# Kernel tuning notes

Hardware: AMD Instinct MI355X
Metric: run time of the kernel (lower is better)

The kernel has to match this reference:

```python
import jax, jax.numpy as jnp
import numpy as np

A, B, I, J, K = 8, 256, 256, 256, 256  # a=batch, b=tokens, i=s-channels, j=c-channels, k=out_dim


def setup_inputs() -> dict:
    key = jax.random.key(0)
    k1, k2, k3 = jax.random.split(key, 3)
    input_s = jax.random.normal(k1, (A, B, I), dtype=jnp.float32)
    input_c = jax.random.normal(k2, (B, J), dtype=jnp.float32)
    # learned params: w ~ N(0, 0.02), b zeros (as in build())
    w = jax.random.normal(k3, (I, J, K), dtype=jnp.float32) * 0.02
    b = jnp.zeros((K,), dtype=jnp.float32)
    return {"input_s": input_s, "input_c": input_c, "w": w, "b": b}


def reference(input_s, input_c, w, b):
    # Original: tmp = einsum('abi,ijk->abjk', input_s, w); out = einsum('bj,abjk->abk', input_c, tmp) + b
    # Mathematically identical fused bilinear contraction (avoids the [a,b,j,k] intermediate):
    out = jnp.einsum('abi,bj,ijk->abk', input_s, input_c, w)
    return out + b
```

## Files before the change

### kernel.cpp

```cpp
#include <hip/hip_runtime.h>
#include <hip/hip_bf16.h>

#define A_ 8
#define B_ 256
#define I_ 256
#define J_ 256
#define K_ 256

typedef __attribute__((ext_vector_type(8))) short short8_t;
typedef __attribute__((ext_vector_type(4))) float f32x4_t;

static __device__ __forceinline__ uint pack2bf(float a, float b) {
  float2 f2; f2.x = a; f2.y = b;
  __hip_bfloat162 h2 = __float22bfloat162_rn(f2);
  uint r;
  __builtin_memcpy(&r, &h2, 4);
  return r;
}

static __device__ __forceinline__ ushort f2bf(float f) {
  __hip_bfloat16 h = __float2bfloat16(f);
  ushort us;
  __builtin_memcpy(&us, &h, 2);
  return us;
}

static __device__ __forceinline__ float bf2f(ushort h) {
  uint u = ((uint)h) << 16;
  float f;
  __builtin_memcpy(&f, &u, 4);
  return f;
}

__global__ __launch_bounds__(256) void prepass_c_kernel(
    const float* __restrict__ c, ushort* __restrict__ cbf) {
  const int idx = blockIdx.x * 256 + threadIdx.x;
  const f32x4_t v = *reinterpret_cast<const f32x4_t*>(c + (size_t)idx * 4);
  uint2 r;
  r.x = pack2bf(v[0], v[1]);
  r.y = pack2bf(v[2], v[3]);
  *reinterpret_cast<uint2*>(cbf + (size_t)idx * 4) = r;
}

#define LDK 40

__global__ __launch_bounds__(256, 3) void pass1_kernel(
    const ushort* __restrict__ cbf, const float* __restrict__ w,
    ushort* __restrict__ u) {
  const int i    = blockIdx.x;
  const int k0   = blockIdx.y * 64;
  const int tid  = threadIdx.x;
  const int lane = tid & 63;
  const int wave = tid >> 6;
  const int lrow = lane & 15;
  const int lhi  = lane >> 4;

  __shared__ ushort Bt[2][64][LDK];

  const float* wi = w + (size_t)i * (J_ * K_) + k0;

  const int jp = tid & 15;
  const int kq = tid >> 4;

  const int arow = wave * 64 + lrow;

  f32x4_t acc[4][4];
#pragma unroll
  for (int m = 0; m < 4; m++)
#pragma unroll
    for (int n = 0; n < 4; n++) acc[m][n] = (f32x4_t)(0.0f);

  f32x4_t  bv[2][2];
  short8_t afr[2][4];

#define BGLOB(p, t)                                                         \
  {                                                                         \
    _Pragma("unroll") for (int jj = 0; jj < 2; jj++)                        \
        bv[p][jj] = *reinterpret_cast<const f32x4_t*>(                      \
            wi + (size_t)((t) * 32 + jp * 2 + jj) * K_ + kq * 4);           \
  }
#define ALOAD(p, t)                                                         \
  {                                                                         \
    _Pragma("unroll") for (int m = 0; m < 4; m++)                           \
        afr[p][m] = *reinterpret_cast<const short8_t*>(                     \
            cbf + (size_t)(arow + m * 16) * J_ + (t) * 32 + lhi * 8);       \
  }
#define STOREB(buf, p)                                                      \
  {                                                                         \
    _Pragma("unroll") for (int kk = 0; kk < 4; kk++)                        \
        *reinterpret_cast<uint*>(&Bt[buf][kq * 4 + kk][jp * 2]) =           \
            pack2bf(bv[p][0][kk], bv[p][1][kk]);                            \
  }

  BGLOB(0, 0);
  BGLOB(1, 1);
  ALOAD(0, 0);
  ALOAD(1, 1);
  STOREB(0, 0);
  asm volatile("s_waitcnt lgkmcnt(0)" ::: "memory");
  __builtin_amdgcn_s_barrier();

#pragma unroll
  for (int t = 0; t < 8; ++t) {
    const int cur = t & 1;
    short8_t bfr[4];
#pragma unroll
    for (int n = 0; n < 4; n++)
      bfr[n] = *reinterpret_cast<const short8_t*>(
          &Bt[cur][n * 16 + lrow][lhi * 8]);
    if (t < 6) BGLOB(cur, t + 2);
#pragma unroll
    for (int m = 0; m < 4; m++)
#pragma unroll
      for (int n = 0; n < 4; n++)
        acc[m][n] = __builtin_amdgcn_mfma_f32_16x16x32_bf16(
            afr[cur][m], bfr[n], acc[m][n], 0, 0, 0);
    if (t < 6) ALOAD(cur, t + 2);
    if (t < 7) {
      STOREB(cur ^ 1, cur ^ 1);
      asm volatile("s_waitcnt lgkmcnt(0)" ::: "memory");
      __builtin_amdgcn_s_barrier();
    }
  }
#undef BGLOB
#undef ALOAD
#undef STOREB

#pragma unroll
  for (int m = 0; m < 4; m++) {
    const int brow = wave * 64 + m * 16 + lhi * 4;
#pragma unroll
    for (int n = 0; n < 4; n++) {
      const int kc = k0 + n * 16 + lrow;
      ushort* up = u + ((size_t)brow * I_ + i) * K_ + kc;
#pragma unroll
      for (int r = 0; r < 4; r++)
        up[(size_t)r * (I_ * K_)] = f2bf(acc[m][n][r]);
    }
  }
}

__global__ __launch_bounds__(256) void pass2_kernel(
    const float* __restrict__ s, const ushort* __restrict__ u,
    const float* __restrict__ bias, float* __restrict__ out) {
  const int b   = blockIdx.x;
  const int a0  = blockIdx.y * 4;
  const int tid = threadIdx.x;
  __shared__ float s_l[4][I_];
  __shared__ float red[8][4][K_];

#pragma unroll
  for (int v = 0; v < 4; v++) {
    const int idx = tid + v * 256;
    const int a = idx >> 8, ii = idx & 255;
    s_l[a][ii] = s[((size_t)(a0 + a) * B_ + b) * I_ + ii];
  }
  __syncthreads();

  const int kb = (tid & 31) * 8;
  const int ig = tid >> 5;
  float acc[4][8];
#pragma unroll
  for (int a = 0; a < 4; a++)
#pragma unroll
    for (int q = 0; q < 8; q++) acc[a][q] = 0.0f;

  const ushort* ub = u + ((size_t)b * I_ + ig * 32) * K_ + kb;
  for (int ii = 0; ii < 32; ++ii) {
    const short8_t uv = *reinterpret_cast<const short8_t*>(ub + (size_t)ii * K_);
    float f[8];
#pragma unroll
    for (int q = 0; q < 8; q++) f[q] = bf2f((ushort)uv[q]);
    const int i = ig * 32 + ii;
#pragma unroll
    for (int a = 0; a < 4; a++) {
      const float sa = s_l[a][i];
#pragma unroll
      for (int q = 0; q < 8; q++) acc[a][q] += sa * f[q];
    }
  }

#pragma unroll
  for (int a = 0; a < 4; a++) {
    f32x4_t r0, r1;
#pragma unroll
    for (int q = 0; q < 4; q++) { r0[q] = acc[a][q]; r1[q] = acc[a][4 + q]; }
    *reinterpret_cast<f32x4_t*>(&red[ig][a][kb])     = r0;
    *reinterpret_cast<f32x4_t*>(&red[ig][a][kb + 4]) = r1;
  }
  __syncthreads();

#pragma unroll
  for (int v = 0; v < 4; v++) {
    const int k = tid;
    float sum = 0.0f;
#pragma unroll
    for (int g = 0; g < 8; g++) sum += red[g][v][k];
    out[((size_t)(a0 + v) * B_ + b) * K_ + k] = sum + bias[k];
  }
}

__global__ __launch_bounds__(256) void fallback_kernel(
    const float* __restrict__ s, const float* __restrict__ cmat,
    const float* __restrict__ w, const float* __restrict__ bias,
    float* __restrict__ out) {
  const int b = blockIdx.x;
  const int k = threadIdx.x;
  __shared__ float c_l[J_];
  __shared__ float s_l[A_][I_];
  for (int idx = threadIdx.x; idx < J_; idx += 256) c_l[idx] = cmat[(size_t)b * J_ + idx];
  for (int idx = threadIdx.x; idx < A_ * I_; idx += 256) {
    const int a = idx >> 8;
    const int i = idx & 255;
    s_l[a][i] = s[(size_t)a * (B_ * I_) + (size_t)b * I_ + i];
  }
  __syncthreads();
  float acc[A_];
#pragma unroll
  for (int a = 0; a < A_; a++) acc[a] = 0.0f;
  for (int i = 0; i < I_; i++) {
    const float* wrow = w + (size_t)i * (J_ * K_) + k;
    float inner = 0.0f;
    for (int j = 0; j < J_; j++) inner += c_l[j] * wrow[(size_t)j * K_];
#pragma unroll
    for (int a = 0; a < A_; a++) acc[a] += s_l[a][i] * inner;
  }
#pragma unroll
  for (int a = 0; a < A_; a++)
    out[((size_t)a * B_ + b) * K_ + k] = acc[a] + bias[k];
}

extern "C" void kernel_launch(void* const* d_in, const int* in_sizes, int n_in,
                              void* d_out, int out_size, void* d_ws, size_t ws_size,
                              hipStream_t stream) {
  const float* s    = (const float*)d_in[0];
  const float* cmat = (const float*)d_in[1];
  const float* w    = (const float*)d_in[2];
  const float* bias = (const float*)d_in[3];
  float* out = (float*)d_out;

  const size_t u_elems   = (size_t)B_ * I_ * K_;
  const size_t cbf_elems = (size_t)B_ * J_;
  const size_t need = (u_elems + cbf_elems) * sizeof(ushort);

  if (ws_size >= need) {
    ushort* u   = (ushort*)d_ws;
    ushort* cbf = (ushort*)d_ws + u_elems;
    prepass_c_kernel<<<dim3((B_ * J_) / (256 * 4)), dim3(256), 0, stream>>>(cmat, cbf);
    pass1_kernel<<<dim3(I_, 4), dim3(256), 0, stream>>>(cbf, w, u);
    pass2_kernel<<<dim3(B_, 2), dim3(256), 0, stream>>>(s, u, bias, out);
  } else {
    fallback_kernel<<<dim3(B_), dim3(256), 0, stream>>>(s, cmat, w, bias, out);
  }
}
```

Before: 46.83 us.

## Widen pass1 tile to 128 k-columns with XOR-swizzled LDS and two-phase staging

Pass1 now covers 128 output columns per block instead of 64, which halves the grid and doubles per-wave accumulators (4x8 MFMA tiles). The w slice is staged into a 64KB LDS buffer with an XOR swizzle on 16-byte chunks to avoid bank conflicts. The pipeline changes from an 8-step double buffer to two j-halves, with the second half's loads and stores overlapping compute on the first. This aims to cut the number of times the cbf A-operand is reloaded and to reduce barriers. In exchange it uses more registers and LDS, allows fewer blocks per CU, and leaves only 512 blocks to fill the device.

```diff
diff --git a/kernel.cpp b/kernel.cpp
--- a/kernel.cpp
+++ b/kernel.cpp
@@ -42,97 +42,102 @@
   *reinterpret_cast<uint2*>(cbf + (size_t)idx * 4) = r;
 }
 
-#define LDK 40
-
-__global__ __launch_bounds__(256, 3) void pass1_kernel(
+__global__ __launch_bounds__(256, 2) void pass1_kernel(
     const ushort* __restrict__ cbf, const float* __restrict__ w,
     ushort* __restrict__ u) {
   const int i    = blockIdx.x;
-  const int k0   = blockIdx.y * 64;
+  const int kh   = blockIdx.y;
   const int tid  = threadIdx.x;
   const int lane = tid & 63;
   const int wave = tid >> 6;
   const int lrow = lane & 15;
   const int lhi  = lane >> 4;
 
-  __shared__ ushort Bt[2][64][LDK];
-
-  const float* wi = w + (size_t)i * (J_ * K_) + k0;
-
-  const int jp = tid & 15;
-  const int kq = tid >> 4;
-
+  __shared__ __align__(16) char Bt[128 * 512];
+
+  const float* wi = w + (size_t)i * (J_ * K_) + kh * 128;
+
+  const int jp = tid & 63;
+  const int kc = tid >> 6;
   const int arow = wave * 64 + lrow;
 
-  f32x4_t acc[4][4];
+  f32x4_t acc[4][8];
 #pragma unroll
   for (int m = 0; m < 4; m++)
 #pragma unroll
-    for (int n = 0; n < 4; n++) acc[m][n] = (f32x4_t)(0.0f);
-
-  f32x4_t  bv[2][2];
-  short8_t afr[2][4];
-
-#define BGLOB(p, t)                                                         \
+    for (int n = 0; n < 8; n++) acc[m][n] = (f32x4_t)(0.0f);
+
+  f32x4_t sv[8];
+
+#define GLOAD(jh, ko)                                                       \
   {                                                                         \
     _Pragma("unroll") for (int jj = 0; jj < 2; jj++)                        \
-        bv[p][jj] = *reinterpret_cast<const f32x4_t*>(                      \
-            wi + (size_t)((t) * 32 + jp * 2 + jj) * K_ + kq * 4);           \
-  }
-#define ALOAD(p, t)                                                         \
+        _Pragma("unroll") for (int q = 0; q < 4; q++)                       \
+        sv[jj * 4 + q] = *reinterpret_cast<const f32x4_t*>(                 \
+            wi + (size_t)((jh) * 128 + jp * 2 + jj) * K_ + kc * 32 + (ko) + \
+            q * 4);                                                         \
+  }
+#define STORE(jh, ko)                                                       \
   {                                                                         \
+    const int jc  = (jh) * 64 + jp;                                         \
+    const int cid = jc >> 2;                                                \
+    const int wb  = (jc & 3) * 4;                                           \
+    _Pragma("unroll") for (int q = 0; q < 16; q++) {                        \
+      const int k = kc * 32 + (ko) + q;                                     \
+      *reinterpret_cast<uint*>(                                             \
+          Bt + k * 512 + ((cid ^ (q & 7)) * 16) + wb) =                     \
+          pack2bf(sv[(q >> 2)][q & 3], sv[4 + (q >> 2)][q & 3]);            \
+    }                                                                       \
+  }
+#define COMPUTE(jh, kk)                                                     \
+  {                                                                         \
+    short8_t af[4];                                                         \
     _Pragma("unroll") for (int m = 0; m < 4; m++)                           \
-        afr[p][m] = *reinterpret_cast<const short8_t*>(                     \
-            cbf + (size_t)(arow + m * 16) * J_ + (t) * 32 + lhi * 8);       \
-  }
-#define STOREB(buf, p)                                                      \
-  {                                                                         \
-    _Pragma("unroll") for (int kk = 0; kk < 4; kk++)                        \
-        *reinterpret_cast<uint*>(&Bt[buf][kq * 4 + kk][jp * 2]) =           \
-            pack2bf(bv[p][0][kk], bv[p][1][kk]);                            \
-  }
-
-  BGLOB(0, 0);
-  BGLOB(1, 1);
-  ALOAD(0, 0);
-  ALOAD(1, 1);
-  STOREB(0, 0);
-  asm volatile("s_waitcnt lgkmcnt(0)" ::: "memory");
-  __builtin_amdgcn_s_barrier();
-
-#pragma unroll
-  for (int t = 0; t < 8; ++t) {
-    const int cur = t & 1;
-    short8_t bfr[4];
-#pragma unroll
-    for (int n = 0; n < 4; n++)
-      bfr[n] = *reinterpret_cast<const short8_t*>(
-          &Bt[cur][n * 16 + lrow][lhi * 8]);
-    if (t < 6) BGLOB(cur, t + 2);
-#pragma unroll
-    for (int m = 0; m < 4; m++)
-#pragma unroll
-      for (int n = 0; n < 4; n++)
-        acc[m][n] = __builtin_amdgcn_mfma_f32_16x16x32_bf16(
-            afr[cur][m], bfr[n], acc[m][n], 0, 0, 0);
-    if (t < 6) ALOAD(cur, t + 2);
-    if (t < 7) {
-      STOREB(cur ^ 1, cur ^ 1);
-      asm volatile("s_waitcnt lgkmcnt(0)" ::: "memory");
-      __builtin_amdgcn_s_barrier();
-    }
-  }
-#undef BGLOB
-#undef ALOAD
-#undef STOREB
+        af[m] = *reinterpret_cast<const short8_t*>(                         \
+            cbf + (size_t)(arow + m * 16) * J_ + (jh) * 128 + (kk) * 32 +   \
+            lhi * 8);                                                       \
+    short8_t bf[8];                                                         \
+    _Pragma("unroll") for (int n = 0; n < 8; n++) {                         \
+      const int row = n * 16 + lrow;                                        \
+      const int cid = ((jh) * 16 + (kk) * 4 + lhi) ^ (lrow & 7);            \
+      bf[n] = *reinterpret_cast<const short8_t*>(Bt + row * 512 + cid * 16);\
+    }                                                                       \
+    _Pragma("unroll") for (int m = 0; m < 4; m++)                           \
+        _Pragma("unroll") for (int n = 0; n < 8; n++)                       \
+        acc[m][n] = __builtin_amdgcn_mfma_f32_16x16x32_bf16(                \
+            af[m], bf[n], acc[m][n], 0, 0, 0);                              \
+  }
+
+  GLOAD(0, 0);  STORE(0, 0);
+  GLOAD(0, 16); STORE(0, 16);
+  __syncthreads();
+
+  GLOAD(1, 0);
+  COMPUTE(0, 0);
+  COMPUTE(0, 1);
+  STORE(1, 0);
+  GLOAD(1, 16);
+  COMPUTE(0, 2);
+  COMPUTE(0, 3);
+  STORE(1, 16);
+  __syncthreads();
+
+  COMPUTE(1, 0);
+  COMPUTE(1, 1);
+  COMPUTE(1, 2);
+  COMPUTE(1, 3);
+
+#undef GLOAD
+#undef STORE
+#undef COMPUTE
 
 #pragma unroll
   for (int m = 0; m < 4; m++) {
     const int brow = wave * 64 + m * 16 + lhi * 4;
 #pragma unroll
-    for (int n = 0; n < 4; n++) {
-      const int kc = k0 + n * 16 + lrow;
-      ushort* up = u + ((size_t)brow * I_ + i) * K_ + kc;
+    for (int n = 0; n < 8; n++) {
+      const int kc_g = kh * 128 + n * 16 + lrow;
+      ushort* up = u + ((size_t)brow * I_ + i) * K_ + kc_g;
 #pragma unroll
       for (int r = 0; r < 4; r++)
         up[(size_t)r * (I_ * K_)] = f2bf(acc[m][n][r]);
@@ -247,7 +252,7 @@
     ushort* u   = (ushort*)d_ws;
     ushort* cbf = (ushort*)d_ws + u_elems;
     prepass_c_kernel<<<dim3((B_ * J_) / (256 * 4)), dim3(256), 0, stream>>>(cmat, cbf);
-    pass1_kernel<<<dim3(I_, 4), dim3(256), 0, stream>>>(cbf, w, u);
+    pass1_kernel<<<dim3(I_, 2), dim3(256), 0, stream>>>(cbf, w, u);
     pass2_kernel<<<dim3(B_, 2), dim3(256), 0, stream>>>(s, u, bias, out);
   } else {
     fallback_kernel<<<dim3(B_), dim3(256), 0, stream>>>(s, cmat, w, bias, out);
```

New measurement: 46.81 us. Within noise of the previous version (-0.0%).

## Pre-transpose weights to bf16 MFMA layout and drop LDS staging in pass1

Applied to the files above, without the earlier changes.

Adds a prepass that converts the fp32 weight tensor to bf16 and stores it in a fragment-ready interleaved layout. Pass1 can then load B operands straight from global memory without LDS staging, barriers or in-loop conversion, and its occupancy hint is raised. In exchange, the full weight tensor makes an extra round trip through memory, the workspace requirement grows by the size of the bf16 weights, and there is one more kernel launch.

```diff
diff --git a/kernel.cpp b/kernel.cpp
--- a/kernel.cpp
+++ b/kernel.cpp
@@ -9,6 +9,7 @@
 
 typedef __attribute__((ext_vector_type(8))) short short8_t;
 typedef __attribute__((ext_vector_type(4))) float f32x4_t;
+typedef __attribute__((ext_vector_type(4))) uint u32x4_t;
 
 static __device__ __forceinline__ uint pack2bf(float a, float b) {
   float2 f2; f2.x = a; f2.y = b;
@@ -42,27 +43,57 @@
   *reinterpret_cast<uint2*>(cbf + (size_t)idx * 4) = r;
 }
 
-#define LDK 40
-
-__global__ __launch_bounds__(256, 3) void pass1_kernel(
-    const ushort* __restrict__ cbf, const float* __restrict__ w,
+__global__ __launch_bounds__(256, 6) void prepass_w2_kernel(
+    const float* __restrict__ w, ushort* __restrict__ wt2) {
+  const int i   = blockIdx.x;
+  const int jc  = blockIdx.y;
+  const int tid = threadIdx.x;
+  const int jp  = tid & 15;
+  const int ks  = tid >> 4;
+  __shared__ uint T[256][17];
+
+  const float* wi = w + (size_t)i * (J_ * K_);
+
+  const int j = jc * 32 + jp * 2;
+  f32x4_t r0[4], r1[4];
+#pragma unroll
+  for (int q = 0; q < 4; q++) {
+    r0[q] = *reinterpret_cast<const f32x4_t*>(wi + (size_t)j * K_ + ks * 16 + q * 4);
+    r1[q] = *reinterpret_cast<const f32x4_t*>(wi + (size_t)(j + 1) * K_ + ks * 16 + q * 4);
+  }
+#pragma unroll
+  for (int q = 0; q < 4; q++)
+#pragma unroll
+    for (int e = 0; e < 4; e++)
+      T[ks * 16 + q * 4 + e][jp] = pack2bf(r0[q][e], r1[q][e]);
+  __syncthreads();
+
+  const int k = tid;
+#pragma unroll
+  for (int js = 0; js < 4; js++) {
+    u32x4_t vv;
+#pragma unroll
+    for (int p = 0; p < 4; p++) vv[p] = T[k][js * 4 + p];
+    *reinterpret_cast<u32x4_t*>(
+        wt2 + (((size_t)i * 32 + jc * 4 + js) * K_ + k) * 8) = vv;
+  }
+}
+
+__global__ __launch_bounds__(256, 4) void pass1_kernel(
+    const ushort* __restrict__ cbf, const ushort* __restrict__ wt2,
     ushort* __restrict__ u) {
   const int i    = blockIdx.x;
-  const int k0   = blockIdx.y * 64;
+  const int kq   = blockIdx.y;
   const int tid  = threadIdx.x;
   const int lane = tid & 63;
-  const int wave = tid >> 6;
+  const int wv   = tid >> 6;
   const int lrow = lane & 15;
   const int lhi  = lane >> 4;
 
-  __shared__ ushort Bt[2][64][LDK];
-
-  const float* wi = w + (size_t)i * (J_ * K_) + k0;
-
-  const int jp = tid & 15;
-  const int kq = tid >> 4;
-
-  const int arow = wave * 64 + lrow;
+  const int arow = wv * 64 + lrow;
+  const ushort* wbase =
+      wt2 + (size_t)i * (J_ * K_) + ((size_t)(kq * 64 + lrow)) * 8 +
+      (size_t)lhi * (K_ * 8);
 
   f32x4_t acc[4][4];
 #pragma unroll
@@ -70,68 +101,31 @@
 #pragma unroll
     for (int n = 0; n < 4; n++) acc[m][n] = (f32x4_t)(0.0f);
 
-  f32x4_t  bv[2][2];
-  short8_t afr[2][4];
-
-#define BGLOB(p, t)                                                         \
-  {                                                                         \
-    _Pragma("unroll") for (int jj = 0; jj < 2; jj++)                        \
-        bv[p][jj] = *reinterpret_cast<const f32x4_t*>(                      \
-            wi + (size_t)((t) * 32 + jp * 2 + jj) * K_ + kq * 4);           \
-  }
-#define ALOAD(p, t)                                                         \
-  {                                                                         \
-    _Pragma("unroll") for (int m = 0; m < 4; m++)                           \
-        afr[p][m] = *reinterpret_cast<const short8_t*>(                     \
-            cbf + (size_t)(arow + m * 16) * J_ + (t) * 32 + lhi * 8);       \
-  }
-#define STOREB(buf, p)                                                      \
-  {                                                                         \
-    _Pragma("unroll") for (int kk = 0; kk < 4; kk++)                        \
-        *reinterpret_cast<uint*>(&Bt[buf][kq * 4 + kk][jp * 2]) =           \
-            pack2bf(bv[p][0][kk], bv[p][1][kk]);                            \
-  }
-
-  BGLOB(0, 0);
-  BGLOB(1, 1);
-  ALOAD(0, 0);
-  ALOAD(1, 1);
-  STOREB(0, 0);
-  asm volatile("s_waitcnt lgkmcnt(0)" ::: "memory");
-  __builtin_amdgcn_s_barrier();
-
 #pragma unroll
   for (int t = 0; t < 8; ++t) {
-    const int cur = t & 1;
-    short8_t bfr[4];
+    short8_t af[4], bf[4];
+#pragma unroll
+    for (int m = 0; m < 4; m++)
+      af[m] = *reinterpret_cast<const short8_t*>(
+          cbf + (size_t)(arow + m * 16) * J_ + t * 32 + lhi * 8);
 #pragma unroll
     for (int n = 0; n < 4; n++)
-      bfr[n] = *reinterpret_cast<const short8_t*>(
-          &Bt[cur][n * 16 + lrow][lhi * 8]);
-    if (t < 6) BGLOB(cur, t + 2);
+      bf[n] = *reinterpret_cast<const short8_t*>(
+          wbase + ((size_t)t * 4) * (K_ * 8) + (size_t)(n * 16) * 8);
 #pragma unroll
     for (int m = 0; m < 4; m++)
 #pragma unroll
       for (int n = 0; n < 4; n++)
-        acc[m][n] = __builtin_amdgcn_mfma_f32_16x16x32_bf16(
-            afr[cur][m], bfr[n], acc[m][n], 0, 0, 0);
-    if (t < 6) ALOAD(cur, t + 2);
-    if (t < 7) {
-      STOREB(cur ^ 1, cur ^ 1);
-      asm volatile("s_waitcnt lgkmcnt(0)" ::: "memory");
-      __builtin_amdgcn_s_barrier();
-    }
-  }
-#undef BGLOB
-#undef ALOAD
-#undef STOREB
+        acc[m][n] = __builtin_amdgcn_mfma_f32_16x16x32_bf16(af[m], bf[n],
+                                                            acc[m][n], 0, 0, 0);
+  }
 
 #pragma unroll
   for (int m = 0; m < 4; m++) {
-    const int brow = wave * 64 + m * 16 + lhi * 4;
+    const int brow = wv * 64 + m * 16 + lhi * 4;
 #pragma unroll
     for (int n = 0; n < 4; n++) {
-      const int kc = k0 + n * 16 + lrow;
+      const int kc = kq * 64 + n * 16 + lrow;
       ushort* up = u + ((size_t)brow * I_ + i) * K_ + kc;
 #pragma unroll
       for (int r = 0; r < 4; r++)
@@ -240,14 +234,17 @@
   float* out = (float*)d_out;
 
   const size_t u_elems   = (size_t)B_ * I_ * K_;
+  const size_t wt_elems  = (size_t)I_ * J_ * K_;
   const size_t cbf_elems = (size_t)B_ * J_;
-  const size_t need = (u_elems + cbf_elems) * sizeof(ushort);
+  const size_t need = (u_elems + wt_elems + cbf_elems) * sizeof(ushort);
 
   if (ws_size >= need) {
     ushort* u   = (ushort*)d_ws;
-    ushort* cbf = (ushort*)d_ws + u_elems;
+    ushort* wt2 = (ushort*)d_ws + u_elems;
+    ushort* cbf = (ushort*)d_ws + u_elems + wt_elems;
     prepass_c_kernel<<<dim3((B_ * J_) / (256 * 4)), dim3(256), 0, stream>>>(cmat, cbf);
-    pass1_kernel<<<dim3(I_, 4), dim3(256), 0, stream>>>(cbf, w, u);
+    prepass_w2_kernel<<<dim3(I_, 8), dim3(256), 0, stream>>>(w, wt2);
+    pass1_kernel<<<dim3(I_, 4), dim3(256), 0, stream>>>(cbf, wt2, u);
     pass2_kernel<<<dim3(B_, 2), dim3(256), 0, stream>>>(s, u, bias, out);
   } else {
     fallback_kernel<<<dim3(B_), dim3(256), 0, stream>>>(s, cmat, w, bias, out);
```

After: 61.88 us. +32.2%, slower.
